# Optimization experiments

Measured on AMD Instinct MI355X. Metric: run time of the kernel, lower is better.

Reference implementation:

```python
import jax, jax.numpy as jnp
import numpy as np

# dims
B, N, D = 2, 4096, 384
NUM_HEADS, KEY_DIM, VALUE_DIM = 8, 48, 48
TOP_K = 128
IDX_HEADS, IDX_DIM = 2, 32
SCALE = KEY_DIM ** (-0.5)


def setup_inputs() -> dict:
    key = jax.random.key(0)
    ks = jax.random.split(key, 9)
    def xavier(k, shape):
        fan_in, fan_out = shape[0], shape[1]
        lim = (6.0 / (fan_in + fan_out)) ** 0.5
        return jax.random.uniform(k, shape, jnp.float32, -lim, lim)
    return {
        "x": jax.random.normal(ks[0], (B, N, D), jnp.float32),
        # lightning indexer params
        "wq_idx": xavier(ks[1], (D, IDX_HEADS * IDX_DIM)),
        "wk_idx": xavier(ks[2], (D, IDX_DIM)),
        "ww_idx": xavier(ks[3], (D, IDX_HEADS)),
        # attention params (stored as (in, out) for x @ W)
        "wq": xavier(ks[4], (D, NUM_HEADS * KEY_DIM)),
        "wk": xavier(ks[5], (D, KEY_DIM)),
        "wv": xavier(ks[6], (D, VALUE_DIM)),
        "wo": xavier(ks[7], (NUM_HEADS * VALUE_DIM, D)),
    }


def _forward(x, wq_idx, wk_idx, ww_idx, wq, wk, wv, wo):
    b, n, d = x.shape
    # ---- Lightning indexer: I[q,s] = sum_h w[q,h] * relu(qi[q,h] . ki[s]) ----
    qi = (x @ wq_idx).reshape(b, n, IDX_HEADS, IDX_DIM)      # (B,N,Hi,dki)
    ki = x @ wk_idx                                           # (B,N,dki)
    w_idx = x @ ww_idx                                        # (B,N,Hi)
    raw = jax.nn.relu(jnp.einsum('bqhd,bsd->bqhs', qi, ki))   # (B,Nq,Hi,Nk)
    index_scores = jnp.einsum('bqhs,bqh->bqs', raw, w_idx)    # (B,Nq,Nk)

    # ---- MQA projections ----
    q = (x @ wq).reshape(b, n, NUM_HEADS, KEY_DIM).transpose(0, 2, 1, 3)  # (B,H,N,dk)
    k = x @ wk                                                # (B,N,dk) single KV head
    v = x @ wv                                                # (B,N,dv)

    # ---- top-k select + gather ----
    kk = min(TOP_K, n)
    _, top_idx = jax.lax.top_k(index_scores, kk)              # (B,Nq,k)
    bidx = jnp.arange(b)[:, None, None]
    sel_k = k[bidx, top_idx]                                  # (B,Nq,k,dk)
    sel_v = v[bidx, top_idx]                                  # (B,Nq,k,dv)

    # ---- sparse attention over selected keys ----
    attn = jnp.einsum('bhqd,bqkd->bhqk', q, sel_k) * SCALE    # (B,H,Nq,k)
    probs = jax.nn.softmax(attn, axis=-1)
    out = jnp.einsum('bhqk,bqkd->bhqd', probs, sel_v)         # (B,H,Nq,dv)
    out = out.transpose(0, 2, 1, 3).reshape(b, n, NUM_HEADS * VALUE_DIM)
    return out @ wo                                           # (B,N,D)


def reference(x, wq_idx, wk_idx, ww_idx, wq, wk, wv, wo):
    return _forward(x, wq_idx, wk_idx, ww_idx, wq, wk, wv, wo)
```

## Files before the change

kernel.cpp:

```cpp
#include <hip/hip_runtime.h>
#include <math.h>

#define NB 2
#define NSEQ 4096
#define DMODEL 384
#define NH 8
#define DKQ 48
#define DV 48
#define TOPK 128
#define NQ (NB*NSEQ)

#define QKV_COLS 480
#define C_Q 0
#define C_K 384
#define C_V 432
#define IDX_COLS 128
#define P_QI 0
#define P_KI 64
#define P_W  96
#define ATT_SCALE 0.14433756729740643f

typedef double v4d  __attribute__((ext_vector_type(4)));
typedef float  f32x4 __attribute__((ext_vector_type(4)));
typedef short  s16x8 __attribute__((ext_vector_type(8)));

__device__ inline void bsplit(float v, unsigned short& h, unsigned short& l) {
    unsigned hb = __float_as_uint(v);
    unsigned short hi = (unsigned short)((hb + 0x7FFFu + ((hb >> 16) & 1u)) >> 16);
    float hf = __uint_as_float(((unsigned)hi) << 16);
    float r = v - hf;
    unsigned rb = __float_as_uint(r);
    unsigned short lo = (unsigned short)((rb + 0x7FFFu + ((rb >> 16) & 1u)) >> 16);
    h = hi; l = lo;
}

__global__ void k_split(const float* __restrict__ x,
                        unsigned short* __restrict__ xhi, unsigned short* __restrict__ xlo) {
    int i = blockIdx.x * 256 + threadIdx.x;
    if (i < NQ * DMODEL) {
        unsigned short h, l;
        bsplit(x[i], h, l);
        xhi[i] = h; xlo[i] = l;
    }
}

__global__ void k_concat(const float* __restrict__ wq_idx, const float* __restrict__ wk_idx,
                         const float* __restrict__ ww_idx, const float* __restrict__ wq,
                         const float* __restrict__ wk, const float* __restrict__ wv,
                         const float* __restrict__ wo,
                         unsigned short* __restrict__ WqT_hi, unsigned short* __restrict__ WqT_lo,
                         unsigned short* __restrict__ WoT_hi, unsigned short* __restrict__ WoT_lo,
                         float* __restrict__ Wi_cat) {
    int i = blockIdx.x * 256 + threadIdx.x;
    const int NQK = QKV_COLS * DMODEL;
    const int NWO = DMODEL * DMODEL;
    if (i < NQK) {
        int n = i / DMODEL, k = i % DMODEL;
        float v;
        if (n < 384)      v = wq[(size_t)k*384 + n];
        else if (n < 432) v = wk[(size_t)k*48 + (n-384)];
        else              v = wv[(size_t)k*48 + (n-432)];
        unsigned short h, l; bsplit(v, h, l);
        WqT_hi[i] = h; WqT_lo[i] = l;
    } else if (i < NQK + NWO) {
        int j = i - NQK;
        int n = j / DMODEL, k = j % DMODEL;
        float v = wo[(size_t)k*384 + n];
        unsigned short h, l; bsplit(v, h, l);
        WoT_hi[j] = h; WoT_lo[j] = l;
    } else if (i < NQK + NWO + DMODEL*IDX_COLS) {
        int j = i - NQK - NWO;
        int d = j / IDX_COLS, c = j % IDX_COLS;
        float v;
        if (c < 64)       v = wq_idx[d*64 + c];
        else if (c < 96)  v = wk_idx[d*32 + (c-64)];
        else if (c < 98)  v = ww_idx[d*2 + (c-96)];
        else              v = 0.f;
        Wi_cat[j] = v;
    }
}

#define GLDK 40
__global__ __launch_bounds__(256) void k_gemm_mfma(
        const unsigned short* __restrict__ Ahi, const unsigned short* __restrict__ Alo,
        const unsigned short* __restrict__ Bhi, const unsigned short* __restrict__ Blo,
        float* __restrict__ C, int N, int ldc) {
    __shared__ unsigned short At[2][128][GLDK];
    __shared__ unsigned short Bt[2][64][GLDK];
    const int t = threadIdx.x;
    const int lane = t & 63, wid = t >> 6;
    const int row0 = blockIdx.y * 128, col0 = blockIdx.x * 64;
    const int ml = lane & 15, kq = lane >> 4;
    const int wm = (wid & 1) * 64, wn = (wid >> 1) * 32;

    unsigned short mv = (unsigned short)(__float_as_uint((float)(ml + 1)) >> 16);
    unsigned short one = 0x3F80;
    s16x8 pa, pb;
    #pragma unroll
    for (int j = 0; j < 8; j++) { pa[j] = (short)mv; pb[j] = (short)one; }
    f32x4 zf = (f32x4){0.f, 0.f, 0.f, 0.f};
    f32x4 rowp = __builtin_amdgcn_mfma_f32_16x16x32_bf16(pa, pb, zf, 0, 0, 0);
    f32x4 colp = __builtin_amdgcn_mfma_f32_16x16x32_bf16(pb, pa, zf, 0, 0, 0);
    int rowm[4], colm[4];
    #pragma unroll
    for (int r = 0; r < 4; r++) {
        rowm[r] = (((int)(rowp[r] * 0.03125f + 0.5f)) - 1) & 15;
        colm[r] = (((int)(colp[r] * 0.03125f + 0.5f)) - 1) & 15;
    }

    f32x4 acc[4][2];
    #pragma unroll
    for (int mt = 0; mt < 4; mt++)
        #pragma unroll
        for (int nt = 0; nt < 2; nt++) acc[mt][nt] = zf;

    for (int k0 = 0; k0 < DMODEL; k0 += 32) {
        #pragma unroll
        for (int i = 0; i < 4; i++) {
            int ch = t + 256*i;
            int arr = ch >> 9, rem = ch & 511;
            int r = rem >> 2, p = rem & 3;
            const unsigned short* src = arr ? Alo : Ahi;
            *(int4*)&At[arr][r][p*8] = *(const int4*)(src + (size_t)(row0 + r)*DMODEL + k0 + p*8);
        }
        #pragma unroll
        for (int i = 0; i < 2; i++) {
            int ch = t + 256*i;
            int arr = ch >> 8, rem = ch & 255;
            int r = rem >> 2, p = rem & 3;
            const unsigned short* src = arr ? Blo : Bhi;
            int gc = col0 + r;
            int4 v = {0, 0, 0, 0};
            if (gc < N) v = *(const int4*)(src + (size_t)gc*DMODEL + k0 + p*8);
            *(int4*)&Bt[arr][r][p*8] = v;
        }
        __syncthreads();
        s16x8 af[4][2], bfr[2][2];
        #pragma unroll
        for (int mt = 0; mt < 4; mt++)
            #pragma unroll
            for (int h = 0; h < 2; h++)
                af[mt][h] = *(const s16x8*)&At[h][wm + mt*16 + ml][kq*8];
        #pragma unroll
        for (int nt = 0; nt < 2; nt++)
            #pragma unroll
            for (int h = 0; h < 2; h++)
                bfr[nt][h] = *(const s16x8*)&Bt[h][wn + nt*16 + ml][kq*8];
        #pragma unroll
        for (int mt = 0; mt < 4; mt++)
            #pragma unroll
            for (int nt = 0; nt < 2; nt++) {
                acc[mt][nt] = __builtin_amdgcn_mfma_f32_16x16x32_bf16(af[mt][0], bfr[nt][0], acc[mt][nt], 0, 0, 0);
                acc[mt][nt] = __builtin_amdgcn_mfma_f32_16x16x32_bf16(af[mt][0], bfr[nt][1], acc[mt][nt], 0, 0, 0);
                acc[mt][nt] = __builtin_amdgcn_mfma_f32_16x16x32_bf16(af[mt][1], bfr[nt][0], acc[mt][nt], 0, 0, 0);
            }
        __syncthreads();
    }
    #pragma unroll
    for (int mt = 0; mt < 4; mt++)
        #pragma unroll
        for (int nt = 0; nt < 2; nt++)
            #pragma unroll
            for (int r = 0; r < 4; r++) {
                int rr = row0 + wm + mt*16 + rowm[r];
                int cc = col0 + wn + nt*16 + colm[r];
                if (cc < N) C[(size_t)rr*ldc + cc] = acc[mt][nt][r];
            }
}

__global__ __launch_bounds__(256) void k_proj64(const float* __restrict__ A,
                                                const float* __restrict__ W,
                                                double* __restrict__ P) {
    __shared__ float At[16][32];
    __shared__ float Bt[16][IDX_COLS];
    const int t  = threadIdx.x;
    const int tx = t & 15;
    const int ty = t >> 4;
    const int row0 = blockIdx.x * 32;
    double acc[2][8] = {};

    for (int k0 = 0; k0 < DMODEL; k0 += 16) {
        if (t < 128) {
            int m = t >> 2, kc = t & 3;
            float4 a = *(const float4*)(A + (size_t)(row0 + m)*DMODEL + k0 + kc*4);
            At[kc*4+0][m] = a.x; At[kc*4+1][m] = a.y;
            At[kc*4+2][m] = a.z; At[kc*4+3][m] = a.w;
        }
        for (int i = 0; i < 2; i++) {
            int lin = t + i*256;
            int kk = lin >> 5, c4 = lin & 31;
            float4 b = *(const float4*)(W + (size_t)(k0+kk)*IDX_COLS + c4*4);
            *(float4*)&Bt[kk][c4*4] = b;
        }
        __syncthreads();
        for (int kk = 0; kk < 16; kk++) {
            float a2[2], b8[8];
            a2[0] = At[kk][ty*2]; a2[1] = At[kk][ty*2+1];
            *(float4*)&b8[0] = *(const float4*)&Bt[kk][tx*8];
            *(float4*)&b8[4] = *(const float4*)&Bt[kk][tx*8+4];
            for (int i = 0; i < 2; i++)
                for (int j = 0; j < 8; j++)
                    acc[i][j] += (double)a2[i] * (double)b8[j];
        }
        __syncthreads();
    }
    for (int i = 0; i < 2; i++)
        for (int j = 0; j < 8; j++)
            P[(size_t)(row0 + ty*2 + i)*IDX_COLS + tx*8 + j] = acc[i][j];
}

__global__ __launch_bounds__(256) void k_score_mfma(const double* __restrict__ P,
                                                    unsigned int* __restrict__ K32,
                                                    unsigned int* __restrict__ L32,
                                                    int qstart) {
    __shared__ double A0[32][33];
    __shared__ double A1[32][33];
    __shared__ double Bk[32][129];
    __shared__ double wsh[2][32];
    const int t = threadIdx.x;
    const int lane = t & 63;
    const int wid = t >> 6;
    const int g0 = qstart + blockIdx.y * 32;
    const int b  = g0 / NSEQ;
    const int s0 = blockIdx.x * 128;

    for (int i = 0; i < 8; i++) {
        int lin = t + i*256;
        int q = lin >> 6, c = lin & 63;
        double v = P[(size_t)(g0 + q)*IDX_COLS + P_QI + c];
        if (c < 32) A0[c][q] = v; else A1[c-32][q] = v;
    }
    for (int i = 0; i < 16; i++) {
        int lin = t + i*256;
        int s = lin >> 5, c = lin & 31;
        Bk[c][s] = P[(size_t)(b*NSEQ + s0 + s)*IDX_COLS + P_KI + c];
    }
    if (t < 64) wsh[t & 1][t >> 1] = P[(size_t)(g0 + (t >> 1))*IDX_COLS + P_W + (t & 1)];

    const int qw = (wid & 1) * 16;
    const int sw = (wid >> 1) * 64;
    const int ml = lane & 15;
    const int kl = lane >> 4;

    v4d zero = (v4d){0.0, 0.0, 0.0, 0.0};
    v4d rowp = __builtin_amdgcn_mfma_f64_16x16x4f64((double)(ml+1), 1.0, zero, 0, 0, 0);
    v4d colp = __builtin_amdgcn_mfma_f64_16x16x4f64(1.0, (double)(ml+1), zero, 0, 0, 0);
    int rowm[4], colm[4];
    #pragma unroll
    for (int r = 0; r < 4; r++) {
        rowm[r] = (((int)(rowp[r] * 0.25 + 0.5)) - 1) & 15;
        colm[r] = (((int)(colp[r] * 0.25 + 0.5)) - 1) & 15;
    }

    __syncthreads();

    v4d acc0[4], acc1[4];
    #pragma unroll
    for (int st = 0; st < 4; st++) { acc0[st] = zero; acc1[st] = zero; }

    #pragma unroll
    for (int k4 = 0; k4 < 8; k4++) {
        int k = k4*4 + kl;
        double a0 = A0[k][qw + ml];
        double a1 = A1[k][qw + ml];
        #pragma unroll
        for (int st = 0; st < 4; st++) {
            double bb = Bk[k][sw + st*16 + ml];
            acc0[st] = __builtin_amdgcn_mfma_f64_16x16x4f64(a0, bb, acc0[st], 0, 0, 0);
            acc1[st] = __builtin_amdgcn_mfma_f64_16x16x4f64(a1, bb, acc1[st], 0, 0, 0);
        }
    }

    #pragma unroll
    for (int reg = 0; reg < 4; reg++) {
        int q = qw + rowm[reg];
        double w0 = wsh[0][q], w1 = wsh[1][q];
        #pragma unroll
        for (int st = 0; st < 4; st++) {
            double sc = w0 * fmax(acc0[st][reg], 0.0) + w1 * fmax(acc1[st][reg], 0.0);
            size_t oidx = (size_t)(blockIdx.y*32 + q)*NSEQ + s0 + sw + st*16 + colm[reg];
            unsigned long long bb = (unsigned long long)__double_as_longlong(sc);
            unsigned long long u = (bb & 0x8000000000000000ULL) ? ~bb : (bb | 0x8000000000000000ULL);
            K32[oidx] = (unsigned int)(u >> 32);
            L32[oidx] = (unsigned int)u;
        }
    }
}

__global__ __launch_bounds__(256) void k_topk(const unsigned int* __restrict__ K32,
                                              const unsigned int* __restrict__ L32,
                                              int* __restrict__ IDX, int qstart) {
    __shared__ unsigned int hist[4][256];
    __shared__ unsigned int wred[4];
    __shared__ unsigned int s_b, s_need, s_flag, s_cnt, s_n;
    __shared__ unsigned int CK[512];
    __shared__ int CI[512];
    const int t = threadIdx.x, lane = t & 63;
    const int wid = t >> 6;
    const int q = blockIdx.x;
    const unsigned int* krow = K32 + (size_t)q * NSEQ;
    const unsigned int* lrow = L32 + (size_t)q * NSEQ;
    int* orow = IDX + (size_t)(qstart + q) * TOPK;

    unsigned int kr[16];
    #pragma unroll
    for (int jj = 0; jj < 4; jj++) {
        uint4 v = *(const uint4*)(krow + (t*4 + 1024*jj));
        kr[jj*4+0] = v.x; kr[jj*4+1] = v.y; kr[jj*4+2] = v.z; kr[jj*4+3] = v.w;
    }
    unsigned int mymax = kr[0];
    #pragma unroll
    for (int j = 1; j < 16; j++) mymax = kr[j] > mymax ? kr[j] : mymax;
    const unsigned int p16 = mymax >> 16;

    unsigned int Tw = 0;
    #pragma unroll
    for (int bit = 15; bit >= 0; --bit) {
        unsigned int trial = Tw | (1u << bit);
        if (__popcll(__ballot(p16 >= trial)) >= 32) Tw = trial;
    }
    if (lane == 0) wred[wid] = Tw;
    if (t == 0) { s_cnt = 0; s_n = 0; s_need = TOPK; s_flag = 0; }
    __syncthreads();
    unsigned int T16 = wred[0];
    T16 = wred[1] < T16 ? wred[1] : T16;
    T16 = wred[2] < T16 ? wred[2] : T16;
    T16 = wred[3] < T16 ? wred[3] : T16;

    #pragma unroll
    for (int j = 0; j < 16; j++) {
        if ((kr[j] >> 16) >= T16) {
            unsigned int pos = atomicAdd(&s_n, 1u);
            if (pos < 512u) { CK[pos] = kr[j]; CI[pos] = (j >> 2)*1024 + t*4 + (j & 3); }
        }
    }
    __syncthreads();
    const unsigned int n = s_n;

    if (n <= 512u) {
        if (wid == 0) {
            unsigned int ck[8]; bool cv[8];
            #pragma unroll
            for (int e = 0; e < 8; e++) {
                int id = lane + e*64;
                cv[e] = (unsigned int)id < n;
                ck[e] = cv[e] ? CK[id] : 0u;
            }
            unsigned int T = 0;
            for (int bit = 31; bit >= 0; --bit) {
                unsigned int trial = T | (1u << bit);
                unsigned int c = 0;
                #pragma unroll
                for (int e = 0; e < 8; e++)
                    c += (unsigned int)__popcll(__ballot(cv[e] && ck[e] >= trial));
                if (c >= (unsigned int)TOPK) T = trial;
            }
            unsigned int G = 0, E = 0;
            #pragma unroll
            for (int e = 0; e < 8; e++) {
                G += (unsigned int)__popcll(__ballot(cv[e] && ck[e] > T));
                E += (unsigned int)__popcll(__ballot(cv[e] && ck[e] == T));
            }
            const unsigned int need = (unsigned int)TOPK - G;
            const unsigned long long ltm = (1ull << lane) - 1ull;

            unsigned int cbase = 0;
            #pragma unroll
            for (int e = 0; e < 8; e++) {
                bool em = cv[e] && ck[e] > T;
                unsigned long long m = __ballot(em);
                if (em) orow[cbase + __popcll(m & ltm)] = CI[lane + e*64];
                cbase += (unsigned int)__popcll(m);
            }
            if (E == need) {
                #pragma unroll
                for (int e = 0; e < 8; e++) {
                    bool em = cv[e] && ck[e] == T;
                    unsigned long long m = __ballot(em);
                    if (em) orow[cbase + __popcll(m & ltm)] = CI[lane + e*64];
                    cbase += (unsigned int)__popcll(m);
                }
            } else {
                unsigned int lo[8]; bool tv[8];
                #pragma unroll
                for (int e = 0; e < 8; e++) {
                    tv[e] = cv[e] && ck[e] == T;
                    lo[e] = tv[e] ? lrow[CI[lane + e*64]] : 0u;
                }
                unsigned int L = 0;
                for (int bit = 31; bit >= 0; --bit) {
                    unsigned int trial = L | (1u << bit);
                    unsigned int c = 0;
                    #pragma unroll
                    for (int e = 0; e < 8; e++)
                        c += (unsigned int)__popcll(__ballot(tv[e] && lo[e] >= trial));
                    if (c >= need) L = trial;
                }
                unsigned int G2 = 0;
                #pragma unroll
                for (int e = 0; e < 8; e++)
                    G2 += (unsigned int)__popcll(__ballot(tv[e] && lo[e] > L));
                #pragma unroll
                for (int e = 0; e < 8; e++) {
                    bool em = tv[e] && lo[e] > L;
                    unsigned long long m = __ballot(em);
                    if (em) orow[cbase + __popcll(m & ltm)] = CI[lane + e*64];
                    cbase += (unsigned int)__popcll(m);
                }
                const unsigned int need3 = need - G2;
                unsigned int r = 0;
                for (int bit = 11; bit >= 0; --bit) {
                    unsigned int trial = r | (1u << bit);
                    unsigned int c = 0;
                    #pragma unroll
                    for (int e = 0; e < 8; e++)
                        c += (unsigned int)__popcll(__ballot(tv[e] && lo[e] == L &&
                                 (unsigned int)CI[lane + e*64] <= trial));
                    if (c <= need3) r = trial;
                }
                #pragma unroll
                for (int e = 0; e < 8; e++) {
                    int idv = CI[lane + e*64];
                    bool em = tv[e] && lo[e] == L && (unsigned int)idv <= r;
                    unsigned long long m = __ballot(em);
                    if (em) orow[cbase + __popcll(m & ltm)] = idv;
                    cbase += (unsigned int)__popcll(m);
                }
            }
        }
        return;
    }

    unsigned int amask = 0;
    #pragma unroll
    for (int j = 0; j < 16; j++)
        if ((kr[j] >> 16) >= T16) amask |= (1u << j);

    auto clearhist = [&]() {
        #pragma unroll
        for (int w = 0; w < 4; w++) hist[w][t] = 0;
        __syncthreads();
    };
    auto decide = [&]() {
        if (wid == 0) {
            unsigned int c[4];
            #pragma unroll
            for (int k2 = 0; k2 < 4; k2++)
                c[k2] = hist[0][lane*4+k2] + hist[1][lane*4+k2]
                      + hist[2][lane*4+k2] + hist[3][lane*4+k2];
            unsigned int run = c[0] + c[1] + c[2] + c[3];
            #pragma unroll
            for (int d2 = 1; d2 < 64; d2 <<= 1) {
                unsigned int v = __shfl_down(run, d2, 64);
                if (lane + d2 < 64) run += v;
            }
            unsigned int need = s_need;
            unsigned int Sb[5];
            Sb[0] = run; Sb[1] = run - c[0]; Sb[2] = Sb[1] - c[1];
            Sb[3] = Sb[2] - c[2]; Sb[4] = Sb[3] - c[3];
            #pragma unroll
            for (int j = 0; j < 4; j++) {
                if (Sb[j] >= need && Sb[j+1] < need) {
                    s_b = (unsigned int)(lane*4 + j);
                    s_need = need - Sb[j+1];
                    s_flag = (need - Sb[j+1] == c[j]) ? 1u : 0u;
                }
            }
        }
        __syncthreads();
    };

    #pragma unroll 1
    for (int stage = 0; stage < 2; ++stage) {
        #pragma unroll 1
        for (int level = 0; level < 4; ++level) {
            const int sh = 24 - 8*level;
            clearhist();
            #pragma unroll
            for (int j = 0; j < 16; j++) {
                if ((amask >> j) & 1u)
                    atomicAdd(&hist[wid][(kr[j] >> sh) & 255u], 1u);
            }
            __syncthreads();
            decide();
            const unsigned int bstar = s_b;

            if (s_flag) {
                #pragma unroll
                for (int j = 0; j < 16; j++) {
                    if (((amask >> j) & 1u) && (((kr[j] >> sh) & 255u) >= bstar))
                        orow[atomicAdd(&s_cnt, 1u)] = (j >> 2)*1024 + t*4 + (j & 3);
                }
                return;
            }
            unsigned int nm = 0;
            #pragma unroll
            for (int j = 0; j < 16; j++) {
                if ((amask >> j) & 1u) {
                    unsigned int d = (kr[j] >> sh) & 255u;
                    if (d > bstar) orow[atomicAdd(&s_cnt, 1u)] = (j >> 2)*1024 + t*4 + (j & 3);
                    else if (d == bstar) nm |= (1u << j);
                }
            }
            amask = nm;
        }
        if (stage == 0) {
            #pragma unroll
            for (int jj = 0; jj < 4; jj++) {
                if ((amask >> (jj*4)) & 0xFu) {
                    uint4 v = *(const uint4*)(lrow + (t*4 + 1024*jj));
                    kr[jj*4+0] = v.x; kr[jj*4+1] = v.y; kr[jj*4+2] = v.z; kr[jj*4+3] = v.w;
                }
            }
        }
    }

    const unsigned int needF = s_need;
    unsigned int base = 0;
    #pragma unroll 1
    for (int jj = 0; jj < 4; jj++) {
        unsigned int m4 = (amask >> (jj*4)) & 0xFu;
        unsigned int cnt = __popc(m4);
        unsigned int inc = cnt;
        #pragma unroll
        for (int d2 = 1; d2 < 64; d2 <<= 1) {
            unsigned int v = __shfl_up(inc, d2, 64);
            if (lane >= d2) inc += v;
        }
        if (lane == 63) wred[wid] = inc;
        __syncthreads();
        unsigned int woff = 0;
        for (int w2 = 0; w2 < wid; w2++) woff += wred[w2];
        unsigned int T = wred[0] + wred[1] + wred[2] + wred[3];
        unsigned int p = base + woff + inc - cnt;
        #pragma unroll
        for (int c = 0; c < 4; c++) {
            if ((m4 >> c) & 1u) {
                if (p < needF) orow[atomicAdd(&s_cnt, 1u)] = jj*1024 + t*4 + c;
                p++;
            }
        }
        base += T;
        __syncthreads();
    }
}

#define KVP 52
__global__ __launch_bounds__(256) void k_attn_qk(const float* __restrict__ Y,
                                                 const int* __restrict__ IDX,
                                                 float* __restrict__ Pr) {
    __shared__ float Ks[TOPK][KVP];
    __shared__ float qsh[NH*DKQ];
    __shared__ int   idxs[TOPK];
    const int g = blockIdx.x;
    const int b = g / NSEQ;
    const int t = threadIdx.x;

    if (t < TOPK) idxs[t] = IDX[(size_t)g*TOPK + t];
    for (int i = t; i < NH*DKQ; i += 256) qsh[i] = Y[(size_t)g*QKV_COLS + C_Q + i];
    __syncthreads();
    #pragma unroll
    for (int i = 0; i < 6; i++) {
        int e = t + 256*i;
        int j = e / 12, p = e % 12;
        const float* src = Y + (size_t)(b*NSEQ + idxs[j])*QKV_COLS + C_K;
        *(float4*)&Ks[j][p*4] = *(const float4*)(src + p*4);
    }
    __syncthreads();

    const int h  = t >> 5;
    const int j0 = t & 31;
    float lo[4] = {0.f, 0.f, 0.f, 0.f};
    #pragma unroll
    for (int c = 0; c < 12; c++) {
        float4 qv = *(const float4*)&qsh[h*DKQ + c*4];
        #pragma unroll
        for (int i = 0; i < 4; i++) {
            float4 kv = *(const float4*)&Ks[j0 + 32*i][c*4];
            lo[i] += qv.x*kv.x + qv.y*kv.y + qv.z*kv.z + qv.w*kv.w;
        }
    }
    #pragma unroll
    for (int i = 0; i < 4; i++) lo[i] *= ATT_SCALE;
    float m = fmaxf(fmaxf(lo[0], lo[1]), fmaxf(lo[2], lo[3]));
    for (int d = 16; d >= 1; d >>= 1) m = fmaxf(m, __shfl_xor(m, d, 64));
    float e0[4], sum = 0.f;
    #pragma unroll
    for (int i = 0; i < 4; i++) { e0[i] = __expf(lo[i] - m); sum += e0[i]; }
    for (int d = 16; d >= 1; d >>= 1) sum += __shfl_xor(sum, d, 64);
    float inv = 1.0f / sum;
    #pragma unroll
    for (int i = 0; i < 4; i++)
        Pr[(size_t)g*(NH*TOPK) + h*TOPK + j0 + 32*i] = e0[i] * inv;
}

__global__ __launch_bounds__(256) void k_attn_pv(const float* __restrict__ Y,
                                                 const int* __restrict__ IDX,
                                                 const float* __restrict__ Pr,
                                                 unsigned short* __restrict__ ctx_hi,
                                                 unsigned short* __restrict__ ctx_lo) {
    __shared__ float Vs[TOPK][KVP];
    __shared__ float prs[NH*TOPK];
    __shared__ int   idxs[TOPK];
    const int g = blockIdx.x;
    const int b = g / NSEQ;
    const int t = threadIdx.x;

    if (t < TOPK) idxs[t] = IDX[(size_t)g*TOPK + t];
    *(float4*)&prs[t*4] = *(const float4*)(Pr + (size_t)g*(NH*TOPK) + t*4);
    __syncthreads();
    #pragma unroll
    for (int i = 0; i < 6; i++) {
        int e = t + 256*i;
        int j = e / 12, p = e % 12;
        const float* src = Y + (size_t)(b*NSEQ + idxs[j])*QKV_COLS + C_V;
        *(float4*)&Vs[j][p*4] = *(const float4*)(src + p*4);
    }
    __syncthreads();

    for (int o = t; o < NH*DV; o += 256) {
        int hh = o / DV, dd = o % DV;
        float acc = 0.f;
        #pragma unroll
        for (int jc = 0; jc < 32; jc++) {
            float4 pv = *(const float4*)&prs[hh*TOPK + jc*4];
            acc += pv.x*Vs[jc*4+0][dd] + pv.y*Vs[jc*4+1][dd]
                 + pv.z*Vs[jc*4+2][dd] + pv.w*Vs[jc*4+3][dd];
        }
        unsigned short h, l;
        bsplit(acc, h, l);
        ctx_hi[(size_t)g*(NH*DV) + o] = h;
        ctx_lo[(size_t)g*(NH*DV) + o] = l;
    }
}

extern "C" void kernel_launch(void* const* d_in, const int* in_sizes, int n_in,
                              void* d_out, int out_size, void* d_ws, size_t ws_size,
                              hipStream_t stream) {
    const float* x      = (const float*)d_in[0];
    const float* wq_idx = (const float*)d_in[1];
    const float* wk_idx = (const float*)d_in[2];
    const float* ww_idx = (const float*)d_in[3];
    const float* wq     = (const float*)d_in[4];
    const float* wk     = (const float*)d_in[5];
    const float* wv     = (const float*)d_in[6];
    const float* wo     = (const float*)d_in[7];
    float* out = (float*)d_out;
    char*  ws  = (char*)d_ws;

    size_t off = 0;
    auto carve = [&](size_t bytes) { size_t o = off; off = (off + bytes + 255) & ~(size_t)255; return o; };
    size_t oWqh = carve((size_t)QKV_COLS*DMODEL*2);
    size_t oWql = carve((size_t)QKV_COLS*DMODEL*2);
    size_t oWoh = carve((size_t)DMODEL*DMODEL*2);
    size_t oWol = carve((size_t)DMODEL*DMODEL*2);
    size_t oWi  = carve((size_t)DMODEL*IDX_COLS*4);
    size_t oXh  = carve((size_t)NQ*DMODEL*2);
    size_t oXl  = carve((size_t)NQ*DMODEL*2);
    size_t oY   = carve((size_t)NQ*QKV_COLS*4);
    size_t oP   = carve((size_t)NQ*IDX_COLS*8);
    size_t oIdx = carve((size_t)NQ*TOPK*4);
    size_t oPr  = carve((size_t)NQ*NH*TOPK*4);
    size_t oCh  = carve((size_t)NQ*NH*DV*2);
    size_t oCl  = carve((size_t)NQ*NH*DV*2);
    size_t oKL  = off;

    int QC = NSEQ;
    while (QC > 32 && oKL + (size_t)QC*NSEQ*8 > ws_size) QC >>= 1;

    unsigned short* WqT_hi = (unsigned short*)(ws + oWqh);
    unsigned short* WqT_lo = (unsigned short*)(ws + oWql);
    unsigned short* WoT_hi = (unsigned short*)(ws + oWoh);
    unsigned short* WoT_lo = (unsigned short*)(ws + oWol);
    float*  Wi_cat = (float*)(ws + oWi);
    unsigned short* xhi = (unsigned short*)(ws + oXh);
    unsigned short* xlo = (unsigned short*)(ws + oXl);
    float*  Y      = (float*)(ws + oY);
    double* P      = (double*)(ws + oP);
    int*    IDX    = (int*)(ws + oIdx);
    float*  Pr     = (float*)(ws + oPr);
    unsigned short* ctx_hi = (unsigned short*)(ws + oCh);
    unsigned short* ctx_lo = (unsigned short*)(ws + oCl);
    unsigned int* K32 = (unsigned int*)(ws + oKL);
    unsigned int* L32 = (unsigned int*)(ws + oKL + (size_t)QC*NSEQ*4);

    int ncat = QKV_COLS*DMODEL + DMODEL*DMODEL + DMODEL*IDX_COLS;
    k_split<<<(NQ*DMODEL + 255)/256, 256, 0, stream>>>(x, xhi, xlo);
    k_concat<<<(ncat + 255)/256, 256, 0, stream>>>(wq_idx, wk_idx, ww_idx, wq, wk, wv, wo,
                                                   WqT_hi, WqT_lo, WoT_hi, WoT_lo, Wi_cat);
    k_gemm_mfma<<<dim3((QKV_COLS + 63)/64, NQ/128), 256, 0, stream>>>(xhi, xlo, WqT_hi, WqT_lo, Y, QKV_COLS, QKV_COLS);
    k_proj64<<<NQ/32, 256, 0, stream>>>(x, Wi_cat, P);
    for (int qs = 0; qs < NQ; qs += QC) {
        k_score_mfma<<<dim3(NSEQ/128, QC/32), 256, 0, stream>>>(P, K32, L32, qs);
        k_topk<<<QC, 256, 0, stream>>>(K32, L32, IDX, qs);
    }
    k_attn_qk<<<NQ, 256, 0, stream>>>(Y, IDX, Pr);
    k_attn_pv<<<NQ, 256, 0, stream>>>(Y, IDX, Pr, ctx_hi, ctx_lo);
    k_gemm_mfma<<<dim3(DMODEL/64, NQ/128), 256, 0, stream>>>(ctx_hi, ctx_lo, WoT_hi, WoT_lo, out, DMODEL, DMODEL);
}
```

Before: 537.0 us.

## Use 32-bit float score keys for top-k and fuse QK and PV attention kernels

The indexer scores, computed in double, are now rounded to float and stored as a single 32-bit sortable key with nontemporal stores. This removes the low-word array and the second radix stage and tie-break pass in top-k. Ties at float precision are now broken by index, so the selected set may differ from a full double-precision ranking. The QK-softmax and PV attention kernels are merged into one kernel that keeps probabilities in shared memory and gathers K and V rows together, removing the Pr round trip. The query chunk size can now cover both batches in one launch pair.

Result: faster. 481.6 us (-10.3%).

```diff
diff --git a/kernel.cpp b/kernel.cpp
--- a/kernel.cpp
+++ b/kernel.cpp
@@ -211,7 +211,6 @@
 
 __global__ __launch_bounds__(256) void k_score_mfma(const double* __restrict__ P,
                                                     unsigned int* __restrict__ K32,
-                                                    unsigned int* __restrict__ L32,
                                                     int qstart) {
     __shared__ double A0[32][33];
     __shared__ double A1[32][33];
@@ -279,27 +278,25 @@
         for (int st = 0; st < 4; st++) {
             double sc = w0 * fmax(acc0[st][reg], 0.0) + w1 * fmax(acc1[st][reg], 0.0);
             size_t oidx = (size_t)(blockIdx.y*32 + q)*NSEQ + s0 + sw + st*16 + colm[reg];
-            unsigned long long bb = (unsigned long long)__double_as_longlong(sc);
-            unsigned long long u = (bb & 0x8000000000000000ULL) ? ~bb : (bb | 0x8000000000000000ULL);
-            K32[oidx] = (unsigned int)(u >> 32);
-            L32[oidx] = (unsigned int)u;
+            float sf = (float)sc;
+            unsigned int ub = __float_as_uint(sf);
+            unsigned int u = (ub & 0x80000000u) ? ~ub : (ub | 0x80000000u);
+            __builtin_nontemporal_store(u, &K32[oidx]);
         }
     }
 }
 
 __global__ __launch_bounds__(256) void k_topk(const unsigned int* __restrict__ K32,
-                                              const unsigned int* __restrict__ L32,
                                               int* __restrict__ IDX, int qstart) {
-    __shared__ unsigned int hist[4][256];
+    __shared__ unsigned int pool[1024];
     __shared__ unsigned int wred[4];
     __shared__ unsigned int s_b, s_need, s_flag, s_cnt, s_n;
-    __shared__ unsigned int CK[512];
-    __shared__ int CI[512];
+    unsigned int* CK = pool;
+    int* CI = (int*)(pool + 512);
     const int t = threadIdx.x, lane = t & 63;
     const int wid = t >> 6;
     const int q = blockIdx.x;
     const unsigned int* krow = K32 + (size_t)q * NSEQ;
-    const unsigned int* lrow = L32 + (size_t)q * NSEQ;
     int* orow = IDX + (size_t)(qstart + q) * TOPK;
 
     unsigned int kr[16];
@@ -339,12 +336,13 @@
 
     if (n <= 512u) {
         if (wid == 0) {
-            unsigned int ck[8]; bool cv[8];
+            unsigned int ck[8]; int ci[8]; bool cv[8];
             #pragma unroll
             for (int e = 0; e < 8; e++) {
                 int id = lane + e*64;
                 cv[e] = (unsigned int)id < n;
                 ck[e] = cv[e] ? CK[id] : 0u;
+                ci[e] = cv[e] ? CI[id] : 0;
             }
             unsigned int T = 0;
             for (int bit = 31; bit >= 0; --bit) {
@@ -369,7 +367,7 @@
             for (int e = 0; e < 8; e++) {
                 bool em = cv[e] && ck[e] > T;
                 unsigned long long m = __ballot(em);
-                if (em) orow[cbase + __popcll(m & ltm)] = CI[lane + e*64];
+                if (em) orow[cbase + __popcll(m & ltm)] = ci[e];
                 cbase += (unsigned int)__popcll(m);
             }
             if (E == need) {
@@ -377,53 +375,25 @@
                 for (int e = 0; e < 8; e++) {
                     bool em = cv[e] && ck[e] == T;
                     unsigned long long m = __ballot(em);
-                    if (em) orow[cbase + __popcll(m & ltm)] = CI[lane + e*64];
+                    if (em) orow[cbase + __popcll(m & ltm)] = ci[e];
                     cbase += (unsigned int)__popcll(m);
                 }
             } else {
-                unsigned int lo[8]; bool tv[8];
-                #pragma unroll
-                for (int e = 0; e < 8; e++) {
-                    tv[e] = cv[e] && ck[e] == T;
-                    lo[e] = tv[e] ? lrow[CI[lane + e*64]] : 0u;
-                }
-                unsigned int L = 0;
-                for (int bit = 31; bit >= 0; --bit) {
-                    unsigned int trial = L | (1u << bit);
-                    unsigned int c = 0;
-                    #pragma unroll
-                    for (int e = 0; e < 8; e++)
-                        c += (unsigned int)__popcll(__ballot(tv[e] && lo[e] >= trial));
-                    if (c >= need) L = trial;
-                }
-                unsigned int G2 = 0;
-                #pragma unroll
-                for (int e = 0; e < 8; e++)
-                    G2 += (unsigned int)__popcll(__ballot(tv[e] && lo[e] > L));
-                #pragma unroll
-                for (int e = 0; e < 8; e++) {
-                    bool em = tv[e] && lo[e] > L;
-                    unsigned long long m = __ballot(em);
-                    if (em) orow[cbase + __popcll(m & ltm)] = CI[lane + e*64];
-                    cbase += (unsigned int)__popcll(m);
-                }
-                const unsigned int need3 = need - G2;
                 unsigned int r = 0;
                 for (int bit = 11; bit >= 0; --bit) {
                     unsigned int trial = r | (1u << bit);
                     unsigned int c = 0;
                     #pragma unroll
                     for (int e = 0; e < 8; e++)
-                        c += (unsigned int)__popcll(__ballot(tv[e] && lo[e] == L &&
-                                 (unsigned int)CI[lane + e*64] <= trial));
-                    if (c <= need3) r = trial;
+                        c += (unsigned int)__popcll(__ballot(cv[e] && ck[e] == T &&
+                                 (unsigned int)ci[e] <= trial));
+                    if (c <= need) r = trial;
                 }
                 #pragma unroll
                 for (int e = 0; e < 8; e++) {
-                    int idv = CI[lane + e*64];
-                    bool em = tv[e] && lo[e] == L && (unsigned int)idv <= r;
+                    bool em = cv[e] && ck[e] == T && (unsigned int)ci[e] <= r;
                     unsigned long long m = __ballot(em);
-                    if (em) orow[cbase + __popcll(m & ltm)] = idv;
+                    if (em) orow[cbase + __popcll(m & ltm)] = ci[e];
                     cbase += (unsigned int)__popcll(m);
                 }
             }
@@ -436,6 +406,7 @@
     for (int j = 0; j < 16; j++)
         if ((kr[j] >> 16) >= T16) amask |= (1u << j);
 
+    unsigned int (*hist)[256] = (unsigned int (*)[256])pool;
     auto clearhist = [&]() {
         #pragma unroll
         for (int w = 0; w < 4; w++) hist[w][t] = 0;
@@ -471,48 +442,36 @@
     };
 
     #pragma unroll 1
-    for (int stage = 0; stage < 2; ++stage) {
-        #pragma unroll 1
-        for (int level = 0; level < 4; ++level) {
-            const int sh = 24 - 8*level;
-            clearhist();
+    for (int level = 0; level < 4; ++level) {
+        const int sh = 24 - 8*level;
+        clearhist();
+        #pragma unroll
+        for (int j = 0; j < 16; j++) {
+            if ((amask >> j) & 1u)
+                atomicAdd(&hist[wid][(kr[j] >> sh) & 255u], 1u);
+        }
+        __syncthreads();
+        decide();
+        const unsigned int bstar = s_b;
+
+        if (s_flag) {
             #pragma unroll
             for (int j = 0; j < 16; j++) {
-                if ((amask >> j) & 1u)
-                    atomicAdd(&hist[wid][(kr[j] >> sh) & 255u], 1u);
-            }
-            __syncthreads();
-            decide();
-            const unsigned int bstar = s_b;
-
-            if (s_flag) {
-                #pragma unroll
-                for (int j = 0; j < 16; j++) {
-                    if (((amask >> j) & 1u) && (((kr[j] >> sh) & 255u) >= bstar))
-                        orow[atomicAdd(&s_cnt, 1u)] = (j >> 2)*1024 + t*4 + (j & 3);
-                }
-                return;
-            }
-            unsigned int nm = 0;
-            #pragma unroll
-            for (int j = 0; j < 16; j++) {
-                if ((amask >> j) & 1u) {
-                    unsigned int d = (kr[j] >> sh) & 255u;
-                    if (d > bstar) orow[atomicAdd(&s_cnt, 1u)] = (j >> 2)*1024 + t*4 + (j & 3);
-                    else if (d == bstar) nm |= (1u << j);
-                }
-            }
-            amask = nm;
-        }
-        if (stage == 0) {
-            #pragma unroll
-            for (int jj = 0; jj < 4; jj++) {
-                if ((amask >> (jj*4)) & 0xFu) {
-                    uint4 v = *(const uint4*)(lrow + (t*4 + 1024*jj));
-                    kr[jj*4+0] = v.x; kr[jj*4+1] = v.y; kr[jj*4+2] = v.z; kr[jj*4+3] = v.w;
-                }
-            }
-        }
+                if (((amask >> j) & 1u) && (((kr[j] >> sh) & 255u) >= bstar))
+                    orow[atomicAdd(&s_cnt, 1u)] = (j >> 2)*1024 + t*4 + (j & 3);
+            }
+            return;
+        }
+        unsigned int nm = 0;
+        #pragma unroll
+        for (int j = 0; j < 16; j++) {
+            if ((amask >> j) & 1u) {
+                unsigned int d = (kr[j] >> sh) & 255u;
+                if (d > bstar) orow[atomicAdd(&s_cnt, 1u)] = (j >> 2)*1024 + t*4 + (j & 3);
+                else if (d == bstar) nm |= (1u << j);
+            }
+        }
+        amask = nm;
     }
 
     const unsigned int needF = s_need;
@@ -545,61 +504,13 @@
     }
 }
 
-#define KVP 52
-__global__ __launch_bounds__(256) void k_attn_qk(const float* __restrict__ Y,
-                                                 const int* __restrict__ IDX,
-                                                 float* __restrict__ Pr) {
-    __shared__ float Ks[TOPK][KVP];
+#define KVR 100
+__global__ __launch_bounds__(256) void k_attn(const float* __restrict__ Y,
+                                              const int* __restrict__ IDX,
+                                              unsigned short* __restrict__ ctx_hi,
+                                              unsigned short* __restrict__ ctx_lo) {
+    __shared__ float KV[TOPK][KVR];
     __shared__ float qsh[NH*DKQ];
-    __shared__ int   idxs[TOPK];
-    const int g = blockIdx.x;
-    const int b = g / NSEQ;
-    const int t = threadIdx.x;
-
-    if (t < TOPK) idxs[t] = IDX[(size_t)g*TOPK + t];
-    for (int i = t; i < NH*DKQ; i += 256) qsh[i] = Y[(size_t)g*QKV_COLS + C_Q + i];
-    __syncthreads();
-    #pragma unroll
-    for (int i = 0; i < 6; i++) {
-        int e = t + 256*i;
-        int j = e / 12, p = e % 12;
-        const float* src = Y + (size_t)(b*NSEQ + idxs[j])*QKV_COLS + C_K;
-        *(float4*)&Ks[j][p*4] = *(const float4*)(src + p*4);
-    }
-    __syncthreads();
-
-    const int h  = t >> 5;
-    const int j0 = t & 31;
-    float lo[4] = {0.f, 0.f, 0.f, 0.f};
-    #pragma unroll
-    for (int c = 0; c < 12; c++) {
-        float4 qv = *(const float4*)&qsh[h*DKQ + c*4];
-        #pragma unroll
-        for (int i = 0; i < 4; i++) {
-            float4 kv = *(const float4*)&Ks[j0 + 32*i][c*4];
-            lo[i] += qv.x*kv.x + qv.y*kv.y + qv.z*kv.z + qv.w*kv.w;
-        }
-    }
-    #pragma unroll
-    for (int i = 0; i < 4; i++) lo[i] *= ATT_SCALE;
-    float m = fmaxf(fmaxf(lo[0], lo[1]), fmaxf(lo[2], lo[3]));
-    for (int d = 16; d >= 1; d >>= 1) m = fmaxf(m, __shfl_xor(m, d, 64));
-    float e0[4], sum = 0.f;
-    #pragma unroll
-    for (int i = 0; i < 4; i++) { e0[i] = __expf(lo[i] - m); sum += e0[i]; }
-    for (int d = 16; d >= 1; d >>= 1) sum += __shfl_xor(sum, d, 64);
-    float inv = 1.0f / sum;
-    #pragma unroll
-    for (int i = 0; i < 4; i++)
-        Pr[(size_t)g*(NH*TOPK) + h*TOPK + j0 + 32*i] = e0[i] * inv;
-}
-
-__global__ __launch_bounds__(256) void k_attn_pv(const float* __restrict__ Y,
-                                                 const int* __restrict__ IDX,
-                                                 const float* __restrict__ Pr,
-                                                 unsigned short* __restrict__ ctx_hi,
-                                                 unsigned short* __restrict__ ctx_lo) {
-    __shared__ float Vs[TOPK][KVP];
     __shared__ float prs[NH*TOPK];
     __shared__ int   idxs[TOPK];
     const int g = blockIdx.x;
@@ -607,15 +518,41 @@
     const int t = threadIdx.x;
 
     if (t < TOPK) idxs[t] = IDX[(size_t)g*TOPK + t];
-    *(float4*)&prs[t*4] = *(const float4*)(Pr + (size_t)g*(NH*TOPK) + t*4);
+    for (int i = t; i < NH*DKQ; i += 256) qsh[i] = Y[(size_t)g*QKV_COLS + C_Q + i];
     __syncthreads();
     #pragma unroll
-    for (int i = 0; i < 6; i++) {
+    for (int i = 0; i < 12; i++) {
         int e = t + 256*i;
-        int j = e / 12, p = e % 12;
-        const float* src = Y + (size_t)(b*NSEQ + idxs[j])*QKV_COLS + C_V;
-        *(float4*)&Vs[j][p*4] = *(const float4*)(src + p*4);
-    }
+        int j = e / 24, p = e % 24;
+        const float* src = Y + (size_t)(b*NSEQ + idxs[j])*QKV_COLS + C_K;
+        *(float4*)&KV[j][p*4] = *(const float4*)(src + p*4);
+    }
+    __syncthreads();
+
+    const int h  = t >> 5;
+    const int j0 = t & 31;
+    float lo[4] = {0.f, 0.f, 0.f, 0.f};
+    #pragma unroll
+    for (int c = 0; c < 12; c++) {
+        float4 qv = *(const float4*)&qsh[h*DKQ + c*4];
+        #pragma unroll
+        for (int i = 0; i < 4; i++) {
+            float4 kv = *(const float4*)&KV[j0 + 32*i][c*4];
+            lo[i] += qv.x*kv.x + qv.y*kv.y + qv.z*kv.z + qv.w*kv.w;
+        }
+    }
+    #pragma unroll
+    for (int i = 0; i < 4; i++) lo[i] *= ATT_SCALE;
+    float m = fmaxf(fmaxf(lo[0], lo[1]), fmaxf(lo[2], lo[3]));
+    for (int d = 16; d >= 1; d >>= 1) m = fmaxf(m, __shfl_xor(m, d, 64));
+    float e0[4], sum = 0.f;
+    #pragma unroll
+    for (int i = 0; i < 4; i++) { e0[i] = __expf(lo[i] - m); sum += e0[i]; }
+    for (int d = 16; d >= 1; d >>= 1) sum += __shfl_xor(sum, d, 64);
+    float inv = 1.0f / sum;
+    #pragma unroll
+    for (int i = 0; i < 4; i++)
+        prs[h*TOPK + j0 + 32*i] = e0[i] * inv;
     __syncthreads();
 
     for (int o = t; o < NH*DV; o += 256) {
@@ -624,13 +561,13 @@
         #pragma unroll
         for (int jc = 0; jc < 32; jc++) {
             float4 pv = *(const float4*)&prs[hh*TOPK + jc*4];
-            acc += pv.x*Vs[jc*4+0][dd] + pv.y*Vs[jc*4+1][dd]
-                 + pv.z*Vs[jc*4+2][dd] + pv.w*Vs[jc*4+3][dd];
-        }
-        unsigned short h, l;
-        bsplit(acc, h, l);
-        ctx_hi[(size_t)g*(NH*DV) + o] = h;
-        ctx_lo[(size_t)g*(NH*DV) + o] = l;
+            acc += pv.x*KV[jc*4+0][48+dd] + pv.y*KV[jc*4+1][48+dd]
+                 + pv.z*KV[jc*4+2][48+dd] + pv.w*KV[jc*4+3][48+dd];
+        }
+        unsigned short ch, cl;
+        bsplit(acc, ch, cl);
+        ctx_hi[(size_t)g*(NH*DV) + o] = ch;
+        ctx_lo[(size_t)g*(NH*DV) + o] = cl;
     }
 }
 
@@ -660,13 +597,12 @@
     size_t oY   = carve((size_t)NQ*QKV_COLS*4);
     size_t oP   = carve((size_t)NQ*IDX_COLS*8);
     size_t oIdx = carve((size_t)NQ*TOPK*4);
-    size_t oPr  = carve((size_t)NQ*NH*TOPK*4);
     size_t oCh  = carve((size_t)NQ*NH*DV*2);
     size_t oCl  = carve((size_t)NQ*NH*DV*2);
     size_t oKL  = off;
 
-    int QC = NSEQ;
-    while (QC > 32 && oKL + (size_t)QC*NSEQ*8 > ws_size) QC >>= 1;
+    int QC = NQ;
+    while (QC > 32 && oKL + (size_t)QC*NSEQ*4 > ws_size) QC >>= 1;
 
     unsigned short* WqT_hi = (unsigned short*)(ws + oWqh);
     unsigned short* WqT_lo = (unsigned short*)(ws + oWql);
@@ -678,11 +614,9 @@
     float*  Y      = (float*)(ws + oY);
     double* P      = (double*)(ws + oP);
     int*    IDX    = (int*)(ws + oIdx);
-    float*  Pr     = (float*)(ws + oPr);
     unsigned short* ctx_hi = (unsigned short*)(ws + oCh);
     unsigned short* ctx_lo = (unsigned short*)(ws + oCl);
     unsigned int* K32 = (unsigned int*)(ws + oKL);
-    unsigned int* L32 = (unsigned int*)(ws + oKL + (size_t)QC*NSEQ*4);
 
     int ncat = QKV_COLS*DMODEL + DMODEL*DMODEL + DMODEL*IDX_COLS;
     k_split<<<(NQ*DMODEL + 255)/256, 256, 0, stream>>>(x, xhi, xlo);
@@ -691,10 +625,9 @@
     k_gemm_mfma<<<dim3((QKV_COLS + 63)/64, NQ/128), 256, 0, stream>>>(xhi, xlo, WqT_hi, WqT_lo, Y, QKV_COLS, QKV_COLS);
     k_proj64<<<NQ/32, 256, 0, stream>>>(x, Wi_cat, P);
     for (int qs = 0; qs < NQ; qs += QC) {
-        k_score_mfma<<<dim3(NSEQ/128, QC/32), 256, 0, stream>>>(P, K32, L32, qs);
-        k_topk<<<QC, 256, 0, stream>>>(K32, L32, IDX, qs);
-    }
-    k_attn_qk<<<NQ, 256, 0, stream>>>(Y, IDX, Pr);
-    k_attn_pv<<<NQ, 256, 0, stream>>>(Y, IDX, Pr, ctx_hi, ctx_lo);
+        k_score_mfma<<<dim3(NSEQ/128, QC/32), 256, 0, stream>>>(P, K32, qs);
+        k_topk<<<QC, 256, 0, stream>>>(K32, IDX, qs);
+    }
+    k_attn<<<NQ, 256, 0, stream>>>(Y, IDX, ctx_hi, ctx_lo);
     k_gemm_mfma<<<dim3(DMODEL/64, NQ/128), 256, 0, stream>>>(ctx_hi, ctx_lo, WoT_hi, WoT_lo, out, DMODEL, DMODEL);
 }
```
